# Performance work log

Hardware: AMD Instinct MI355X
Metric: run time of the kernel (lower is better)

The kernel has to match this reference:

```python
import jax, jax.numpy as jnp
import numpy as np

B = 524288
H = 64  # hidden_dim
D = 1   # input_dim


def setup_inputs() -> dict:
    key = jax.random.key(0)
    ks = jax.random.split(key, 16)
    s = 0.05
    inp = {
        "gradients": jax.random.normal(ks[0], (B, D), jnp.float32),
        "parameters": jax.random.normal(ks[1], (B, D), jnp.float32),
        "momentum": jax.random.normal(ks[2], (B, D), jnp.float32),
        "h0": jax.random.normal(ks[3], (B, H), jnp.float32),
        "c0": jax.random.normal(ks[4], (B, H), jnp.float32),
        # input_processor: Linear(3D->H), ReLU, Linear(H->H)
        "W1": jax.random.normal(ks[5], (H, 3 * D), jnp.float32) * s,
        "b1": jax.random.normal(ks[6], (H,), jnp.float32) * s,
        "W2": jax.random.normal(ks[7], (H, H), jnp.float32) * s,
        "b2": jax.random.normal(ks[8], (H,), jnp.float32) * s,
        # LSTM cell (PyTorch layout: gates stacked i,f,g,o -> 4H rows)
        "W_ih": jax.random.normal(ks[9], (4 * H, H), jnp.float32) * s,
        "W_hh": jax.random.normal(ks[10], (4 * H, H), jnp.float32) * s,
        "b_ih": jax.random.normal(ks[11], (4 * H,), jnp.float32) * s,
        "b_hh": jax.random.normal(ks[12], (4 * H,), jnp.float32) * s,
        # output_layer: Linear(H->D)
        "W_out": jax.random.normal(ks[13], (D, H), jnp.float32) * s,
        "b_out": jax.random.normal(ks[14], (D,), jnp.float32) * s,
    }
    return inp


def reference(gradients, parameters, momentum, h0, c0,
              W1, b1, W2, b2, W_ih, W_hh, b_ih, b_hh, W_out, b_out):
    # momentum update
    m = 0.9 * momentum + gradients                      # [B, D]
    feats = jnp.concatenate([gradients, parameters, m], axis=-1)  # [B, 3D]
    # small MLP
    x = jax.nn.relu(feats @ W1.T + b1) @ W2.T + b2      # [B, H]
    # single-step LSTM cell, PyTorch gate order i, f, g, o
    gates = x @ W_ih.T + b_ih + h0 @ W_hh.T + b_hh      # [B, 4H]
    i, f, g, o = jnp.split(gates, 4, axis=-1)
    c1 = jax.nn.sigmoid(f) * c0 + jax.nn.sigmoid(i) * jnp.tanh(g)
    h1 = jax.nn.sigmoid(o) * jnp.tanh(c1)               # [B, H]
    update = h1 @ W_out.T + b_out                       # [B, D]
    return update
```

## Files before the change

kernel.cpp:

```cpp
#include <hip/hip_runtime.h>
#include <hip/hip_bf16.h>
#include <stdint.h>


typedef __attribute__((ext_vector_type(8))) __bf16  bf16x8;
typedef __attribute__((ext_vector_type(8))) float   f32x8;
typedef __attribute__((ext_vector_type(4))) float   floatx4;

__device__ __forceinline__ unsigned short f2bf_bits(float x){
    unsigned u = __builtin_bit_cast(unsigned, x);
    u = u + 0x7fffu + ((u >> 16) & 1u);
    return (unsigned short)(u >> 16);
}
__device__ __forceinline__ bf16x8 pack8(float4 a, float4 b){
    f32x8 t;
    t[0]=a.x; t[1]=a.y; t[2]=a.z; t[3]=a.w;
    t[4]=b.x; t[5]=b.y; t[6]=b.z; t[7]=b.w;
    return __builtin_convertvector(t, bf16x8);
}

__global__ __launch_bounds__(256) void prep_kernel(
    const float* __restrict__ W2, const float* __restrict__ b2,
    const float* __restrict__ W_ih, const float* __restrict__ W_hh,
    const float* __restrict__ b_ih, const float* __restrict__ b_hh,
    unsigned short* __restrict__ wc, float* __restrict__ biasc)
{
    __shared__ float W2s[64*64];
    __shared__ float b2s[64];
    __shared__ float wihs[16*64];
    const int tid = threadIdx.x;
    const int b   = blockIdx.x;

    for (int i = 0; i < 4; i++){
        int idx = i*1024 + tid*4;
        *(float4*)(W2s + idx) = *(const float4*)(W2 + idx);
    }
    if (tid < 64) b2s[tid] = b2[tid];
    {
        int idx = tid*4;
        *(float4*)(wihs + idx) = *(const float4*)(W_ih + b*16*64 + idx);
    }
    __syncthreads();

    const int nl = tid >> 4;
    const int n  = b*16 + nl;
    const int jg = tid & 15;
    const int j  = jg*4;
    const int T  = n >> 4;

    float a0=0.f, a1=0.f, a2=0.f, a3=0.f;
    for (int h = 0; h < 64; h++){
        float wv = wihs[nl*64 + h];
        const float* w2r = W2s + h*64 + j;
        a0 += wv*w2r[0]; a1 += wv*w2r[1]; a2 += wv*w2r[2]; a3 += wv*w2r[3];
    }
    auto store4 = [&](int k, float v0, float v1, float v2, float v3){
        int s    = k >> 5;
        int lane = ((k >> 3) & 3)*16 + (n & 15);
        int off  = (T*4 + s)*512 + lane*8 + (k & 7);
        ushort4 v; v.x=f2bf_bits(v0); v.y=f2bf_bits(v1); v.z=f2bf_bits(v2); v.w=f2bf_bits(v3);
        *(ushort4*)(wc + off) = v;
    };
    store4(j, a0, a1, a2, a3);
    {
        const float* src = W_hh + n*64 + j;
        store4(64 + j, src[0], src[1], src[2], src[3]);
    }
    if (jg == 0){
        float s = b_ih[n] + b_hh[n];
        for (int h = 0; h < 64; h++) s += wihs[nl*64 + h]*b2s[h];
        biasc[n] = s;
    }
}

__global__ __launch_bounds__(512, 4) void main_kernel(
    const float* __restrict__ grad, const float* __restrict__ param,
    const float* __restrict__ mom,  const float* __restrict__ h0,
    const float* __restrict__ c0,   const float* __restrict__ W1,
    const float* __restrict__ b1,   const float* __restrict__ Wout,
    const float* __restrict__ bout,
    const unsigned short* __restrict__ wc, const float* __restrict__ biasc,
    float* __restrict__ out)
{
    __shared__ __align__(16) unsigned short wc_l[32768];
    __shared__ float  bias_l[256];
    __shared__ float4 w1p_l[64];
    __shared__ float  wout_l[64];

    const int tid  = threadIdx.x;
    const int lane = tid & 63;
    const int w    = tid >> 6;
    const int l15  = lane & 15;
    const int q    = lane >> 4;
    const long row0 = (long)blockIdx.x * 256;

    {
        const float4* src = (const float4*)wc;
        float4*       dst = (float4*)wc_l;
        #pragma unroll
        for (int i = 0; i < 8; i++)
            dst[i*512 + tid] = src[i*512 + tid];
    }
    if (tid < 256){
        float sc = ((tid >> 6) == 2) ? 2.885390082f : -1.442695041f;
        bias_l[tid] = sc * biasc[tid];
    } else if (tid < 320){
        int j = tid - 256;
        w1p_l[j] = make_float4(W1[j*3], W1[j*3+1], W1[j*3+2], b1[j]);
    } else if (tid < 384){
        wout_l[tid - 320] = Wout[tid - 320];
    }

    const long rA0 = row0 + w*32 + l15;
    const long rA1 = rA0 + 16;
    float g0 = grad[rA0], p0 = param[rA0], mo0 = mom[rA0];
    float g1 = grad[rA1], p1 = param[rA1], mo1 = mom[rA1];
    const float* hr0 = h0 + rA0*64;
    float4 ha0 = *(const float4*)(hr0 + q*8);
    float4 hb0 = *(const float4*)(hr0 + q*8 + 4);
    float4 hc0 = *(const float4*)(hr0 + 32 + q*8);
    float4 hd0 = *(const float4*)(hr0 + 32 + q*8 + 4);
    const float* hr1 = h0 + rA1*64;
    float4 ha1 = *(const float4*)(hr1 + q*8);
    float4 hb1 = *(const float4*)(hr1 + q*8 + 4);
    float4 hc1 = *(const float4*)(hr1 + 32 + q*8);
    float4 hd1 = *(const float4*)(hr1 + 32 + q*8 + 4);
    const float bout0 = bout[0];

    __syncthreads();

    float m0 = fmaf(0.9f, mo0, g0);
    float m1 = fmaf(0.9f, mo1, g1);
    f32x8 rlo0, rhi0, rlo1, rhi1;
    #pragma unroll
    for (int jj = 0; jj < 8; jj++){
        float4 wr = w1p_l[q*8 + jj];
        float v0 = fmaf(wr.x, g0, fmaf(wr.y, p0, fmaf(wr.z, m0, wr.w)));
        float v1 = fmaf(wr.x, g1, fmaf(wr.y, p1, fmaf(wr.z, m1, wr.w)));
        rlo0[jj] = v0 > 0.f ? v0 : 0.f;
        rlo1[jj] = v1 > 0.f ? v1 : 0.f;
    }
    #pragma unroll
    for (int jj = 0; jj < 8; jj++){
        float4 wr = w1p_l[32 + q*8 + jj];
        float v0 = fmaf(wr.x, g0, fmaf(wr.y, p0, fmaf(wr.z, m0, wr.w)));
        float v1 = fmaf(wr.x, g1, fmaf(wr.y, p1, fmaf(wr.z, m1, wr.w)));
        rhi0[jj] = v0 > 0.f ? v0 : 0.f;
        rhi1[jj] = v1 > 0.f ? v1 : 0.f;
    }
    bf16x8 a0_0 = __builtin_convertvector(rlo0, bf16x8);
    bf16x8 a1_0 = __builtin_convertvector(rhi0, bf16x8);
    bf16x8 a2_0 = pack8(ha0, hb0);
    bf16x8 a3_0 = pack8(hc0, hd0);
    bf16x8 a0_1 = __builtin_convertvector(rlo1, bf16x8);
    bf16x8 a1_1 = __builtin_convertvector(rhi1, bf16x8);
    bf16x8 a2_1 = pack8(ha1, hb1);
    bf16x8 a3_1 = pack8(hc1, hd1);

    const float* c0b0 = c0 + (row0 + w*32 + q*4)*64 + l15;
    const float* c0b1 = c0 + (row0 + w*32 + 16 + q*4)*64 + l15;

    float red0[4] = {0.f, 0.f, 0.f, 0.f};
    float red1[4] = {0.f, 0.f, 0.f, 0.f};
    const floatx4 zq = {0.f, 0.f, 0.f, 0.f};

    #pragma unroll 1
    for (int jh = 0; jh < 4; ++jh){
        const int jh16 = jh << 4;

        float c00[4], c01[4];
        #pragma unroll
        for (int r = 0; r < 4; ++r){
            c00[r] = c0b0[jh16 + r*64];
            c01[r] = c0b1[jh16 + r*64];
        }

        float bsi = bias_l[jh16 + l15];
        float bsf = bias_l[jh16 + l15 + 64];
        float bsg = bias_l[jh16 + l15 + 128];
        float bso = bias_l[jh16 + l15 + 192];
        float wo  = wout_l[jh16 + l15];

        const unsigned short* cb = wc_l + jh*2048 + lane*8;
        floatx4 xi0, xi1, xf0, xf1, xg0, xg1, xo0, xo1;

        #define GATE(Gofs, d0, d1)                                            \
        {                                                                     \
            bf16x8 t0 = *(const bf16x8*)(cb + (Gofs));                        \
            bf16x8 t1 = *(const bf16x8*)(cb + (Gofs) + 512);                  \
            bf16x8 t2 = *(const bf16x8*)(cb + (Gofs) + 1024);                 \
            bf16x8 t3 = *(const bf16x8*)(cb + (Gofs) + 1536);                 \
            d0 = __builtin_amdgcn_mfma_f32_16x16x32_bf16(a0_0, t0, zq, 0,0,0);\
            d1 = __builtin_amdgcn_mfma_f32_16x16x32_bf16(a0_1, t0, zq, 0,0,0);\
            d0 = __builtin_amdgcn_mfma_f32_16x16x32_bf16(a1_0, t1, d0, 0,0,0);\
            d1 = __builtin_amdgcn_mfma_f32_16x16x32_bf16(a1_1, t1, d1, 0,0,0);\
            d0 = __builtin_amdgcn_mfma_f32_16x16x32_bf16(a2_0, t2, d0, 0,0,0);\
            d1 = __builtin_amdgcn_mfma_f32_16x16x32_bf16(a2_1, t2, d1, 0,0,0);\
            d0 = __builtin_amdgcn_mfma_f32_16x16x32_bf16(a3_0, t3, d0, 0,0,0);\
            d1 = __builtin_amdgcn_mfma_f32_16x16x32_bf16(a3_1, t3, d1, 0,0,0);\
        }
        GATE(0,     xi0, xi1)
        GATE(8192,  xf0, xf1)
        GATE(16384, xg0, xg1)
        GATE(24576, xo0, xo1)
        #undef GATE

        #pragma unroll
        for (int r = 0; r < 4; ++r){
            float ei = __builtin_amdgcn_exp2f(fmaf(-1.442695041f, xi0[r], bsi));
            float iv = __builtin_amdgcn_rcpf(1.0f + ei);
            float ef = __builtin_amdgcn_exp2f(fmaf(-1.442695041f, xf0[r], bsf));
            float fv = __builtin_amdgcn_rcpf(1.0f + ef);
            float eo = __builtin_amdgcn_exp2f(fmaf(-1.442695041f, xo0[r], bso));
            float ov = __builtin_amdgcn_rcpf(1.0f + eo);
            float eg = __builtin_amdgcn_exp2f(fmaf( 2.885390082f, xg0[r], bsg));
            float gv = fmaf(-2.0f, __builtin_amdgcn_rcpf(1.0f + eg), 1.0f);
            float c1 = fmaf(fv, c00[r], iv*gv);
            float ec = __builtin_amdgcn_exp2f(2.885390082f * c1);
            float tv = fmaf(-2.0f, __builtin_amdgcn_rcpf(1.0f + ec), 1.0f);
            red0[r] = fmaf(ov * tv, wo, red0[r]);
        }
        #pragma unroll
        for (int r = 0; r < 4; ++r){
            float ei = __builtin_amdgcn_exp2f(fmaf(-1.442695041f, xi1[r], bsi));
            float iv = __builtin_amdgcn_rcpf(1.0f + ei);
            float ef = __builtin_amdgcn_exp2f(fmaf(-1.442695041f, xf1[r], bsf));
            float fv = __builtin_amdgcn_rcpf(1.0f + ef);
            float eo = __builtin_amdgcn_exp2f(fmaf(-1.442695041f, xo1[r], bso));
            float ov = __builtin_amdgcn_rcpf(1.0f + eo);
            float eg = __builtin_amdgcn_exp2f(fmaf( 2.885390082f, xg1[r], bsg));
            float gv = fmaf(-2.0f, __builtin_amdgcn_rcpf(1.0f + eg), 1.0f);
            float c1 = fmaf(fv, c01[r], iv*gv);
            float ec = __builtin_amdgcn_exp2f(2.885390082f * c1);
            float tv = fmaf(-2.0f, __builtin_amdgcn_rcpf(1.0f + ec), 1.0f);
            red1[r] = fmaf(ov * tv, wo, red1[r]);
        }
    }

    #pragma unroll
    for (int mset = 1; mset < 16; mset <<= 1)
        #pragma unroll
        for (int r = 0; r < 4; r++){
            red0[r] += __shfl_xor(red0[r], mset, 64);
            red1[r] += __shfl_xor(red1[r], mset, 64);
        }

    if (l15 == 0){
        long orow0 = row0 + w*32 + q*4;
        #pragma unroll
        for (int r = 0; r < 4; r++){
            out[orow0 + r]      = red0[r] + bout0;
            out[orow0 + 16 + r] = red1[r] + bout0;
        }
    }
}

extern "C" void kernel_launch(void* const* d_in, const int* in_sizes, int n_in,
                              void* d_out, int out_size, void* d_ws, size_t ws_size,
                              hipStream_t stream)
{
    const float* grad  = (const float*)d_in[0];
    const float* param = (const float*)d_in[1];
    const float* mom   = (const float*)d_in[2];
    const float* h0    = (const float*)d_in[3];
    const float* c0    = (const float*)d_in[4];
    const float* W1    = (const float*)d_in[5];
    const float* b1    = (const float*)d_in[6];
    const float* W2    = (const float*)d_in[7];
    const float* b2    = (const float*)d_in[8];
    const float* W_ih  = (const float*)d_in[9];
    const float* W_hh  = (const float*)d_in[10];
    const float* b_ih  = (const float*)d_in[11];
    const float* b_hh  = (const float*)d_in[12];
    const float* Wout  = (const float*)d_in[13];
    const float* bout  = (const float*)d_in[14];

    unsigned short* wc = (unsigned short*)d_ws;
    float* biasc       = (float*)((char*)d_ws + 65536);

    prep_kernel<<<16, 256, 0, stream>>>(W2, b2, W_ih, W_hh, b_ih, b_hh, wc, biasc);

    const int nblocks = 524288 / 256;
    main_kernel<<<nblocks, 512, 0, stream>>>(grad, param, mom, h0, c0,
                                             W1, b1, Wout, bout, wc, biasc,
                                             (float*)d_out);
}
```

Measured before the change: 314.1 us.

## Coalesce h0 loads via LDS transpose and prefetch c0 with async global-to-LDS

Each block now has 1024 threads and covers 512 rows, so the weight copy into LDS is amortised over twice as many rows. h0 is read with fully coalesced float4 loads, converted to bf16 and staged through a per-wave swizzled LDS region to form the MFMA operands. c0 tiles are streamed into LDS with global_load_lds in a double-buffered prefetch that overlaps with the MFMA and epilogue work, replacing strided scalar loads. In exchange LDS use grows by 64KB per block, which limits occupancy, and the manual waitcnt sequencing is fragile.

```diff
diff --git a/kernel.cpp b/kernel.cpp
--- a/kernel.cpp
+++ b/kernel.cpp
@@ -4,7 +4,9 @@
 
 
 typedef __attribute__((ext_vector_type(8))) __bf16  bf16x8;
+typedef __attribute__((ext_vector_type(4))) __bf16  bf16x4;
 typedef __attribute__((ext_vector_type(8))) float   f32x8;
+typedef __attribute__((ext_vector_type(4))) float   f32x4v;
 typedef __attribute__((ext_vector_type(4))) float   floatx4;
 
 __device__ __forceinline__ unsigned short f2bf_bits(float x){
@@ -12,12 +14,11 @@
     u = u + 0x7fffu + ((u >> 16) & 1u);
     return (unsigned short)(u >> 16);
 }
-__device__ __forceinline__ bf16x8 pack8(float4 a, float4 b){
-    f32x8 t;
-    t[0]=a.x; t[1]=a.y; t[2]=a.z; t[3]=a.w;
-    t[4]=b.x; t[5]=b.y; t[6]=b.z; t[7]=b.w;
-    return __builtin_convertvector(t, bf16x8);
-}
+
+#define GLD_LDS16(gp, lp)                                                     \
+    __builtin_amdgcn_global_load_lds(                                         \
+        (const __attribute__((address_space(1))) void*)(const void*)(gp),     \
+        (__attribute__((address_space(3))) void*)(void*)(lp), 16, 0, 0)
 
 __global__ __launch_bounds__(256) void prep_kernel(
     const float* __restrict__ W2, const float* __restrict__ b2,
@@ -73,7 +74,7 @@
     }
 }
 
-__global__ __launch_bounds__(512, 4) void main_kernel(
+__global__ __launch_bounds__(1024, 4) void main_kernel(
     const float* __restrict__ grad, const float* __restrict__ param,
     const float* __restrict__ mom,  const float* __restrict__ h0,
     const float* __restrict__ c0,   const float* __restrict__ W1,
@@ -83,6 +84,7 @@
     float* __restrict__ out)
 {
     __shared__ __align__(16) unsigned short wc_l[32768];
+    __shared__ __align__(16) unsigned char  region[16*4096];
     __shared__ float  bias_l[256];
     __shared__ float4 w1p_l[64];
     __shared__ float  wout_l[64];
@@ -92,14 +94,15 @@
     const int w    = tid >> 6;
     const int l15  = lane & 15;
     const int q    = lane >> 4;
-    const long row0 = (long)blockIdx.x * 256;
+    const long row0 = (long)blockIdx.x * 512 + w*32;
+    unsigned char* Rb = region + w*4096;
 
     {
         const float4* src = (const float4*)wc;
         float4*       dst = (float4*)wc_l;
         #pragma unroll
-        for (int i = 0; i < 8; i++)
-            dst[i*512 + tid] = src[i*512 + tid];
+        for (int i = 0; i < 4; i++)
+            dst[i*1024 + tid] = src[i*1024 + tid];
     }
     if (tid < 256){
         float sc = ((tid >> 6) == 2) ? 2.885390082f : -1.442695041f;
@@ -111,23 +114,49 @@
         wout_l[tid - 320] = Wout[tid - 320];
     }
 
-    const long rA0 = row0 + w*32 + l15;
-    const long rA1 = rA0 + 16;
-    float g0 = grad[rA0], p0 = param[rA0], mo0 = mom[rA0];
-    float g1 = grad[rA1], p1 = param[rA1], mo1 = mom[rA1];
-    const float* hr0 = h0 + rA0*64;
-    float4 ha0 = *(const float4*)(hr0 + q*8);
-    float4 hb0 = *(const float4*)(hr0 + q*8 + 4);
-    float4 hc0 = *(const float4*)(hr0 + 32 + q*8);
-    float4 hd0 = *(const float4*)(hr0 + 32 + q*8 + 4);
-    const float* hr1 = h0 + rA1*64;
-    float4 ha1 = *(const float4*)(hr1 + q*8);
-    float4 hb1 = *(const float4*)(hr1 + q*8 + 4);
-    float4 hc1 = *(const float4*)(hr1 + 32 + q*8);
-    float4 hd1 = *(const float4*)(hr1 + 32 + q*8 + 4);
+    float4 hv0[4], hv1[4];
+    {
+        const float* base0 = h0 + row0*64;
+        const float* base1 = h0 + (row0+16)*64;
+        #pragma unroll
+        for (int j = 0; j < 4; j++){
+            hv0[j] = *(const float4*)(base0 + (j*64 + lane)*4);
+            hv1[j] = *(const float4*)(base1 + (j*64 + lane)*4);
+        }
+    }
+    float g0 = grad[row0 + l15],      p0 = param[row0 + l15],      mo0 = mom[row0 + l15];
+    float g1 = grad[row0 + 16 + l15], p1 = param[row0 + 16 + l15], mo1 = mom[row0 + 16 + l15];
     const float bout0 = bout[0];
 
+    {
+        const int c    = (lane >> 1) & 7;
+        const int half = lane & 1;
+        const int rb   = lane >> 4;
+        #pragma unroll
+        for (int j = 0; j < 4; j++){
+            int r  = j*4 + rb;
+            int gp = (c + r) & 7;
+            f32x4v t0; t0[0]=hv0[j].x; t0[1]=hv0[j].y; t0[2]=hv0[j].z; t0[3]=hv0[j].w;
+            f32x4v t1; t1[0]=hv1[j].x; t1[1]=hv1[j].y; t1[2]=hv1[j].z; t1[3]=hv1[j].w;
+            *(bf16x4*)(Rb + r*128 + gp*16 + half*8)        = __builtin_convertvector(t0, bf16x4);
+            *(bf16x4*)(Rb + 2048 + r*128 + gp*16 + half*8) = __builtin_convertvector(t1, bf16x4);
+        }
+    }
+    asm volatile("s_waitcnt lgkmcnt(0)" ::: "memory");
+    bf16x8 a2_0 = *(const bf16x8*)(Rb + l15*128 + (((q     + l15) & 7) << 4));
+    bf16x8 a3_0 = *(const bf16x8*)(Rb + l15*128 + (((q + 4 + l15) & 7) << 4));
+    bf16x8 a2_1 = *(const bf16x8*)(Rb + 2048 + l15*128 + (((q     + l15) & 7) << 4));
+    bf16x8 a3_1 = *(const bf16x8*)(Rb + 2048 + l15*128 + (((q + 4 + l15) & 7) << 4));
+
     __syncthreads();
+
+    const int rr = lane >> 2, cc = lane & 3;
+    const float* c0s0 = c0 + (row0 + rr)*64 + cc*4;
+    const float* c0s1 = c0 + (row0 + 16 + rr)*64 + cc*4;
+    GLD_LDS16(c0s0,      Rb);
+    GLD_LDS16(c0s1,      Rb + 1024);
+    GLD_LDS16(c0s0 + 16, Rb + 2048);
+    GLD_LDS16(c0s1 + 16, Rb + 2048 + 1024);
 
     float m0 = fmaf(0.9f, mo0, g0);
     float m1 = fmaf(0.9f, mo1, g1);
@@ -150,92 +179,86 @@
     }
     bf16x8 a0_0 = __builtin_convertvector(rlo0, bf16x8);
     bf16x8 a1_0 = __builtin_convertvector(rhi0, bf16x8);
-    bf16x8 a2_0 = pack8(ha0, hb0);
-    bf16x8 a3_0 = pack8(hc0, hd0);
     bf16x8 a0_1 = __builtin_convertvector(rlo1, bf16x8);
     bf16x8 a1_1 = __builtin_convertvector(rhi1, bf16x8);
-    bf16x8 a2_1 = pack8(ha1, hb1);
-    bf16x8 a3_1 = pack8(hc1, hd1);
-
-    const float* c0b0 = c0 + (row0 + w*32 + q*4)*64 + l15;
-    const float* c0b1 = c0 + (row0 + w*32 + 16 + q*4)*64 + l15;
 
     float red0[4] = {0.f, 0.f, 0.f, 0.f};
     float red1[4] = {0.f, 0.f, 0.f, 0.f};
     const floatx4 zq = {0.f, 0.f, 0.f, 0.f};
 
-    #pragma unroll 1
-    for (int jh = 0; jh < 4; ++jh){
-        const int jh16 = jh << 4;
-
-        float c00[4], c01[4];
-        #pragma unroll
-        for (int r = 0; r < 4; ++r){
-            c00[r] = c0b0[jh16 + r*64];
-            c01[r] = c0b1[jh16 + r*64];
-        }
-
-        float bsi = bias_l[jh16 + l15];
-        float bsf = bias_l[jh16 + l15 + 64];
-        float bsg = bias_l[jh16 + l15 + 128];
-        float bso = bias_l[jh16 + l15 + 192];
-        float wo  = wout_l[jh16 + l15];
-
-        const unsigned short* cb = wc_l + jh*2048 + lane*8;
-        floatx4 xi0, xi1, xf0, xf1, xg0, xg1, xo0, xo1;
-
-        #define GATE(Gofs, d0, d1)                                            \
-        {                                                                     \
-            bf16x8 t0 = *(const bf16x8*)(cb + (Gofs));                        \
-            bf16x8 t1 = *(const bf16x8*)(cb + (Gofs) + 512);                  \
-            bf16x8 t2 = *(const bf16x8*)(cb + (Gofs) + 1024);                 \
-            bf16x8 t3 = *(const bf16x8*)(cb + (Gofs) + 1536);                 \
-            d0 = __builtin_amdgcn_mfma_f32_16x16x32_bf16(a0_0, t0, zq, 0,0,0);\
-            d1 = __builtin_amdgcn_mfma_f32_16x16x32_bf16(a0_1, t0, zq, 0,0,0);\
-            d0 = __builtin_amdgcn_mfma_f32_16x16x32_bf16(a1_0, t1, d0, 0,0,0);\
-            d1 = __builtin_amdgcn_mfma_f32_16x16x32_bf16(a1_1, t1, d1, 0,0,0);\
-            d0 = __builtin_amdgcn_mfma_f32_16x16x32_bf16(a2_0, t2, d0, 0,0,0);\
-            d1 = __builtin_amdgcn_mfma_f32_16x16x32_bf16(a2_1, t2, d1, 0,0,0);\
-            d0 = __builtin_amdgcn_mfma_f32_16x16x32_bf16(a3_0, t3, d0, 0,0,0);\
-            d1 = __builtin_amdgcn_mfma_f32_16x16x32_bf16(a3_1, t3, d1, 0,0,0);\
-        }
-        GATE(0,     xi0, xi1)
-        GATE(8192,  xf0, xf1)
-        GATE(16384, xg0, xg1)
-        GATE(24576, xo0, xo1)
-        #undef GATE
-
-        #pragma unroll
-        for (int r = 0; r < 4; ++r){
-            float ei = __builtin_amdgcn_exp2f(fmaf(-1.442695041f, xi0[r], bsi));
-            float iv = __builtin_amdgcn_rcpf(1.0f + ei);
-            float ef = __builtin_amdgcn_exp2f(fmaf(-1.442695041f, xf0[r], bsf));
-            float fv = __builtin_amdgcn_rcpf(1.0f + ef);
-            float eo = __builtin_amdgcn_exp2f(fmaf(-1.442695041f, xo0[r], bso));
-            float ov = __builtin_amdgcn_rcpf(1.0f + eo);
-            float eg = __builtin_amdgcn_exp2f(fmaf( 2.885390082f, xg0[r], bsg));
-            float gv = fmaf(-2.0f, __builtin_amdgcn_rcpf(1.0f + eg), 1.0f);
-            float c1 = fmaf(fv, c00[r], iv*gv);
-            float ec = __builtin_amdgcn_exp2f(2.885390082f * c1);
-            float tv = fmaf(-2.0f, __builtin_amdgcn_rcpf(1.0f + ec), 1.0f);
-            red0[r] = fmaf(ov * tv, wo, red0[r]);
-        }
-        #pragma unroll
-        for (int r = 0; r < 4; ++r){
-            float ei = __builtin_amdgcn_exp2f(fmaf(-1.442695041f, xi1[r], bsi));
-            float iv = __builtin_amdgcn_rcpf(1.0f + ei);
-            float ef = __builtin_amdgcn_exp2f(fmaf(-1.442695041f, xf1[r], bsf));
-            float fv = __builtin_amdgcn_rcpf(1.0f + ef);
-            float eo = __builtin_amdgcn_exp2f(fmaf(-1.442695041f, xo1[r], bso));
-            float ov = __builtin_amdgcn_rcpf(1.0f + eo);
-            float eg = __builtin_amdgcn_exp2f(fmaf( 2.885390082f, xg1[r], bsg));
-            float gv = fmaf(-2.0f, __builtin_amdgcn_rcpf(1.0f + eg), 1.0f);
-            float c1 = fmaf(fv, c01[r], iv*gv);
-            float ec = __builtin_amdgcn_exp2f(2.885390082f * c1);
-            float tv = fmaf(-2.0f, __builtin_amdgcn_rcpf(1.0f + ec), 1.0f);
-            red1[r] = fmaf(ov * tv, wo, red1[r]);
-        }
-    }
+#define GATE(cb, Gofs, d0, d1)                                                \
+{                                                                             \
+    bf16x8 t0 = *(const bf16x8*)((cb) + (Gofs));                              \
+    bf16x8 t1 = *(const bf16x8*)((cb) + (Gofs) + 512);                        \
+    bf16x8 t2 = *(const bf16x8*)((cb) + (Gofs) + 1024);                       \
+    bf16x8 t3 = *(const bf16x8*)((cb) + (Gofs) + 1536);                       \
+    d0 = __builtin_amdgcn_mfma_f32_16x16x32_bf16(a0_0, t0, zq, 0,0,0);        \
+    d1 = __builtin_amdgcn_mfma_f32_16x16x32_bf16(a0_1, t0, zq, 0,0,0);        \
+    d0 = __builtin_amdgcn_mfma_f32_16x16x32_bf16(a1_0, t1, d0, 0,0,0);        \
+    d1 = __builtin_amdgcn_mfma_f32_16x16x32_bf16(a1_1, t1, d1, 0,0,0);        \
+    d0 = __builtin_amdgcn_mfma_f32_16x16x32_bf16(a2_0, t2, d0, 0,0,0);        \
+    d1 = __builtin_amdgcn_mfma_f32_16x16x32_bf16(a2_1, t2, d1, 0,0,0);        \
+    d0 = __builtin_amdgcn_mfma_f32_16x16x32_bf16(a3_0, t3, d0, 0,0,0);        \
+    d1 = __builtin_amdgcn_mfma_f32_16x16x32_bf16(a3_1, t3, d1, 0,0,0);        \
+}
+
+#define EPILOG(XI, XF, XG, XO, CV, BI, BF, BG, BO, WO, RED)                   \
+    _Pragma("unroll")                                                         \
+    for (int r = 0; r < 4; ++r){                                              \
+        float ei = __builtin_amdgcn_exp2f(fmaf(-1.442695041f, XI[r], BI));    \
+        float iv = __builtin_amdgcn_rcpf(1.0f + ei);                          \
+        float ef = __builtin_amdgcn_exp2f(fmaf(-1.442695041f, XF[r], BF));    \
+        float fv = __builtin_amdgcn_rcpf(1.0f + ef);                          \
+        float eo = __builtin_amdgcn_exp2f(fmaf(-1.442695041f, XO[r], BO));    \
+        float ov = __builtin_amdgcn_rcpf(1.0f + eo);                          \
+        float eg = __builtin_amdgcn_exp2f(fmaf( 2.885390082f, XG[r], BG));    \
+        float gv = fmaf(-2.0f, __builtin_amdgcn_rcpf(1.0f + eg), 1.0f);       \
+        float c1 = fmaf(fv, CV[r], iv*gv);                                    \
+        float ec = __builtin_amdgcn_exp2f(2.885390082f * c1);                 \
+        float tv = fmaf(-2.0f, __builtin_amdgcn_rcpf(1.0f + ec), 1.0f);       \
+        RED[r] = fmaf(ov * tv, WO, RED[r]);                                   \
+    }
+
+#define PHASE(JH, VMCNT_STR, DO_PREFETCH)                                     \
+{                                                                             \
+    const int jh16 = (JH) << 4;                                               \
+    const float bsi = bias_l[jh16 + l15];                                     \
+    const float bsf = bias_l[jh16 + l15 + 64];                                \
+    const float bsg = bias_l[jh16 + l15 + 128];                               \
+    const float bso = bias_l[jh16 + l15 + 192];                               \
+    const float wo  = wout_l[jh16 + l15];                                     \
+    const unsigned short* cbp = wc_l + (JH)*2048 + lane*8;                    \
+    floatx4 xi0,xi1,xf0,xf1,xg0,xg1,xo0,xo1;                                  \
+    GATE(cbp, 0,     xi0, xi1)                                                \
+    GATE(cbp, 8192,  xf0, xf1)                                                \
+    GATE(cbp, 16384, xg0, xg1)                                                \
+    GATE(cbp, 24576, xo0, xo1)                                                \
+    asm volatile("s_waitcnt vmcnt(" VMCNT_STR ")" ::: "memory");              \
+    const float* cbf0 = (const float*)(Rb + ((JH)&1)*2048);                   \
+    const float* cbf1 = (const float*)(Rb + ((JH)&1)*2048 + 1024);            \
+    float c00[4], c01[4];                                                     \
+    _Pragma("unroll")                                                         \
+    for (int r = 0; r < 4; ++r){                                              \
+        c00[r] = cbf0[(q*4+r)*16 + l15];                                      \
+        c01[r] = cbf1[(q*4+r)*16 + l15];                                      \
+    }                                                                         \
+    EPILOG(xi0, xf0, xg0, xo0, c00, bsi, bsf, bsg, bso, wo, red0)             \
+    EPILOG(xi1, xf1, xg1, xo1, c01, bsi, bsf, bsg, bso, wo, red1)             \
+    if (DO_PREFETCH){                                                         \
+        asm volatile("s_waitcnt lgkmcnt(0)" ::: "memory");                    \
+        GLD_LDS16(c0s0 + ((JH)+2)*16, Rb + ((JH)&1)*2048);                    \
+        GLD_LDS16(c0s1 + ((JH)+2)*16, Rb + ((JH)&1)*2048 + 1024);             \
+    }                                                                         \
+}
+
+    PHASE(0, "2", 1)
+    PHASE(1, "2", 1)
+    PHASE(2, "2", 0)
+    PHASE(3, "0", 0)
+
+#undef PHASE
+#undef EPILOG
+#undef GATE
 
     #pragma unroll
     for (int mset = 1; mset < 16; mset <<= 1)
@@ -246,11 +269,11 @@
         }
 
     if (l15 == 0){
-        long orow0 = row0 + w*32 + q*4;
+        long orow = row0 + q*4;
         #pragma unroll
         for (int r = 0; r < 4; r++){
-            out[orow0 + r]      = red0[r] + bout0;
-            out[orow0 + 16 + r] = red1[r] + bout0;
+            out[orow + r]      = red0[r] + bout0;
+            out[orow + 16 + r] = red1[r] + bout0;
         }
     }
 }
@@ -280,8 +303,8 @@
 
     prep_kernel<<<16, 256, 0, stream>>>(W2, b2, W_ih, W_hh, b_ih, b_hh, wc, biasc);
 
-    const int nblocks = 524288 / 256;
-    main_kernel<<<nblocks, 512, 0, stream>>>(grad, param, mom, h0, c0,
-                                             W1, b1, Wout, bout, wc, biasc,
-                                             (float*)d_out);
-}
+    const int nblocks = 524288 / 512;
+    main_kernel<<<nblocks, 1024, 0, stream>>>(grad, param, mom, h0, c0,
+                                              W1, b1, Wout, bout, wc, biasc,
+                                              (float*)d_out);
+}
```

Result: slower. 406.0 us (+29.2%).
